# Kernel tuning notes

Hardware: AMD Instinct MI355X
Metric: run time of the kernel (lower is better)

## Reference

```python
import jax, jax.numpy as jnp
import numpy as np

NUM_EMBEDDINGS = 512
EMBEDDING_DIM = 64
COMMITMENT_COST = 0.25


def setup_inputs() -> dict:
    key = jax.random.key(0)
    k1, k2 = jax.random.split(key)
    inputs = jax.random.normal(k1, (64, 32, 32, EMBEDDING_DIM), dtype=jnp.float32)
    # nn.Embedding weight init: uniform(-1/K, 1/K)
    codebook = jax.random.uniform(
        k2, (NUM_EMBEDDINGS, EMBEDDING_DIM), dtype=jnp.float32,
        minval=-1.0 / NUM_EMBEDDINGS, maxval=1.0 / NUM_EMBEDDINGS)
    return {"inputs": inputs, "codebook": codebook}


def reference(inputs, codebook):
    D = codebook.shape[1]
    K = codebook.shape[0]
    flat = inputs.reshape(-1, D)  # [N, D]
    # Squared euclidean distances (argmin-equivalent to torch.cdist output)
    d2 = (jnp.sum(flat * flat, axis=1, keepdims=True)
          - 2.0 * (flat @ codebook.T)
          + jnp.sum(codebook * codebook, axis=1))  # [N, K]
    idx = jnp.argmin(d2, axis=1)  # [N]
    # Gather codebook rows (== one-hot @ codebook in the original)
    quantized = codebook[idx].reshape(inputs.shape)
    e_latent_loss = jnp.mean((jax.lax.stop_gradient(quantized) - inputs) ** 2)
    q_latent_loss = jnp.mean((quantized - jax.lax.stop_gradient(inputs)) ** 2)
    loss = q_latent_loss + COMMITMENT_COST * e_latent_loss
    # Straight-through estimator
    quantized_st = inputs + jax.lax.stop_gradient(quantized - inputs)
    # Perplexity from code usage histogram (== mean of one-hot encodings)
    n = flat.shape[0]
    avg_probs = jnp.zeros((K,), dtype=jnp.float32).at[idx].add(1.0) / n
    perplexity = jnp.exp(-jnp.sum(avg_probs * jnp.log(avg_probs + 1e-10)))
    encoding_indices = idx[:, None]  # [N, 1] to match torch unsqueeze(1)
    return (loss, quantized_st, perplexity, encoding_indices)
```

## Files before the change

### kernel.cpp

```cpp
#include <hip/hip_runtime.h>
#include <math.h>

#define K_EMB 512
#define DIM 64
#define NVEC 65536
#define OUT_LOSS 0
#define OUT_Q 1
#define OUT_PERP (1 + NVEC * DIM)
#define OUT_IDX (1 + NVEC * DIM + 1)
#define EPS2 1e-4f
#define FIX_CAP 32

typedef __attribute__((ext_vector_type(8))) short short8;
typedef __attribute__((ext_vector_type(4))) float float4v;


__device__ __forceinline__ unsigned short bf16_rn(float f) {
    unsigned u = __float_as_uint(f);
    return (unsigned short)((u + 0x7FFFu + ((u >> 16) & 1u)) >> 16);
}

__device__ __forceinline__ float np_pairwise8_sq(const float* v) {
    float r[8];
#pragma unroll
    for (int j = 0; j < 8; ++j) r[j] = __fmul_rn(v[j], v[j]);
#pragma unroll
    for (int i = 8; i < 64; i += 8) {
#pragma unroll
        for (int j = 0; j < 8; ++j) r[j] = __fadd_rn(r[j], __fmul_rn(v[i + j], v[i + j]));
    }
    return __fadd_rn(__fadd_rn(__fadd_rn(r[0], r[1]), __fadd_rn(r[2], r[3])),
                     __fadd_rn(__fadd_rn(r[4], r[5]), __fadd_rn(r[6], r[7])));
}

__global__ void vq_setup(const float* __restrict__ codebook, float* __restrict__ csq) {
    const int k = threadIdx.x;
    csq[k] = np_pairwise8_sq(codebook + (k << 6));
}

__global__ void vq_frag(const float* __restrict__ codebook, const float* __restrict__ csq,
                        unsigned short* __restrict__ ahi, unsigned short* __restrict__ alo,
                        float4* __restrict__ csqf) {
    const int id = blockIdx.x * 256 + threadIdx.x;
    const int t = id >> 7, step = (id >> 6) & 1, lane = id & 63;
    const int m = t * 16 + (lane & 15);
    const int kb = step * 32 + (lane >> 4) * 8;
    const float* src = codebook + (m << 6) + kb;
    short8 h, l;
#pragma unroll
    for (int j = 0; j < 8; ++j) {
        float f = src[j];
        unsigned short hv = bf16_rn(f);
        float lof = f - __uint_as_float(((unsigned)hv) << 16);
        h[j] = (short)hv;
        l[j] = (short)bf16_rn(lof);
    }
    const int fo = ((t * 2 + step) * 64 + lane) * 8;
    *(short8*)(ahi + fo) = h;
    *(short8*)(alo + fo) = l;
    if (step == 0) {
        const int k0 = t * 16 + (lane >> 4) * 4;
        csqf[t * 64 + lane] = make_float4(csq[k0], csq[k0 + 1], csq[k0 + 2], csq[k0 + 3]);
    }
}

__launch_bounds__(256, 4)
__global__ void vq_main(const float* __restrict__ inputs, const float* __restrict__ codebook,
                        const float* __restrict__ csq, const unsigned short* __restrict__ ahi,
                        const unsigned short* __restrict__ alo, const float4* __restrict__ csqf,
                        unsigned* __restrict__ hist, double* __restrict__ sse,
                        float* __restrict__ out) {
    __shared__ __align__(16) float s_x[128 * 68];
    __shared__ float s_A[128];
    __shared__ unsigned long long s_e[128];
    __shared__ unsigned s_h[512];
    __shared__ int s_fix[FIX_CAP];
    __shared__ int s_nfix;
    __shared__ float s_w[4];

    const int tid = threadIdx.x;
    const int wave = tid >> 6, lane = tid & 63;
    const int blk = blockIdx.x;
    const int vbase = blk * 128;

    if (tid == 0) s_nfix = 0;
    s_h[tid] = 0u; s_h[tid + 256] = 0u;

    {
        const float4* src = (const float4*)(inputs + ((size_t)vbase << 6));
#pragma unroll
        for (int it = 0; it < 8; ++it) {
            float4 v = src[it * 256 + tid];
            const int row = it * 16 + (tid >> 4), col = (tid & 15) * 4;
            *(float4*)&s_x[row * 68 + col] = v;
        }
    }
    __syncthreads();

    if (tid < 128) {
        const float* xr = &s_x[tid * 68];
        s_A[tid] = np_pairwise8_sq(xr);
    }
    __syncthreads();

    short8 bhi[2][2], blo[2][2];
    float Av[2];
#pragma unroll
    for (int vt = 0; vt < 2; ++vt) {
        const int vrow = wave * 32 + vt * 16 + (lane & 15);
        Av[vt] = s_A[vrow];
#pragma unroll
        for (int step = 0; step < 2; ++step) {
            const int kb = step * 32 + (lane >> 4) * 8;
            float4 f0 = *(const float4*)&s_x[vrow * 68 + kb];
            float4 f1 = *(const float4*)&s_x[vrow * 68 + kb + 4];
            const float fs[8] = {f0.x, f0.y, f0.z, f0.w, f1.x, f1.y, f1.z, f1.w};
            short8 h, l;
#pragma unroll
            for (int j = 0; j < 8; ++j) {
                unsigned short hv = bf16_rn(fs[j]);
                float lof = fs[j] - __uint_as_float(((unsigned)hv) << 16);
                h[j] = (short)hv;
                l[j] = (short)bf16_rn(lof);
            }
            bhi[vt][step] = h;
            blo[vt][step] = l;
        }
    }

    unsigned long long e1[2] = {~0ULL, ~0ULL}, e2[2] = {~0ULL, ~0ULL};

#pragma unroll 2
    for (int t = 0; t < 32; ++t) {
        const int fo0 = ((t * 2 + 0) * 64 + lane) * 8;
        const int fo1 = ((t * 2 + 1) * 64 + lane) * 8;
        short8 ah0 = *(const short8*)(ahi + fo0);
        short8 ah1 = *(const short8*)(ahi + fo1);
        short8 al0 = *(const short8*)(alo + fo0);
        short8 al1 = *(const short8*)(alo + fo1);
        float4 cs = csqf[t * 64 + lane];
        const float csr[4] = {cs.x, cs.y, cs.z, cs.w};
#pragma unroll
        for (int vt = 0; vt < 2; ++vt) {
            float4v acc = {0.f, 0.f, 0.f, 0.f};
            acc = __builtin_amdgcn_mfma_f32_16x16x32_bf16(ah0, bhi[vt][0], acc, 0, 0, 0);
            acc = __builtin_amdgcn_mfma_f32_16x16x32_bf16(ah1, bhi[vt][1], acc, 0, 0, 0);
            acc = __builtin_amdgcn_mfma_f32_16x16x32_bf16(ah0, blo[vt][0], acc, 0, 0, 0);
            acc = __builtin_amdgcn_mfma_f32_16x16x32_bf16(ah1, blo[vt][1], acc, 0, 0, 0);
            acc = __builtin_amdgcn_mfma_f32_16x16x32_bf16(al0, bhi[vt][0], acc, 0, 0, 0);
            acc = __builtin_amdgcn_mfma_f32_16x16x32_bf16(al1, bhi[vt][1], acc, 0, 0, 0);
#pragma unroll
            for (int r = 0; r < 4; ++r) {
                float d2 = __fadd_rn(__fsub_rn(Av[vt], __fmul_rn(2.0f, acc[r])), csr[r]);
                const unsigned k = (unsigned)(t * 16 + (lane >> 4) * 4 + r);
                unsigned long long e = ((unsigned long long)__float_as_uint(d2) << 32) | k;
                if (e < e1[vt]) { e2[vt] = e1[vt]; e1[vt] = e; }
                else if (e < e2[vt]) e2[vt] = e;
            }
        }
    }

#pragma unroll
    for (int vt = 0; vt < 2; ++vt) {
#pragma unroll
        for (int off = 16; off <= 32; off <<= 1) {
            unsigned long long o1 = __shfl_xor(e1[vt], off);
            unsigned long long o2 = __shfl_xor(e2[vt], off);
            if (o1 < e1[vt]) { e2[vt] = (e1[vt] < o2) ? e1[vt] : o2; e1[vt] = o1; }
            else if (o1 < e2[vt]) e2[vt] = o1;
        }
        if (lane < 16) {
            const int vloc = wave * 32 + vt * 16 + lane;
            s_e[vloc] = e1[vt];
            float b1 = __uint_as_float((unsigned)(e1[vt] >> 32));
            float b2 = __uint_as_float((unsigned)(e2[vt] >> 32));
            if (__fsub_rn(b2, b1) <= EPS2) {
                int pos = atomicAdd(&s_nfix, 1);
                if (pos < FIX_CAP) s_fix[pos] = vloc;
            }
        }
    }
    __syncthreads();

    {
        int nf = s_nfix; if (nf > FIX_CAP) nf = FIX_CAP;
        for (int f = wave; f < nf; f += 4) {
            const int vloc = s_fix[f];
            const float* xr = &s_x[vloc * 68];
            const float A = s_A[vloc];
            unsigned long long best = ~0ULL;
#pragma unroll 1
            for (int r8 = 0; r8 < 8; ++r8) {
                const int k = lane * 8 + r8;
                const float* c = codebook + (k << 6);
                float p[8] = {0.f, 0.f, 0.f, 0.f, 0.f, 0.f, 0.f, 0.f};
#pragma unroll
                for (int ii = 0; ii < 64; ii += 8)
#pragma unroll
                    for (int j = 0; j < 8; ++j)
                        p[j] = __builtin_fmaf(xr[ii + j], c[ii + j], p[j]);
                float dot = __fadd_rn(__fadd_rn(__fadd_rn(p[0], p[1]), __fadd_rn(p[2], p[3])),
                                      __fadd_rn(__fadd_rn(p[4], p[5]), __fadd_rn(p[6], p[7])));
                float d2 = __fadd_rn(__fsub_rn(A, __fmul_rn(2.0f, dot)), csq[k]);
                unsigned long long e = ((unsigned long long)__float_as_uint(d2) << 32) | (unsigned)k;
                if (e < best) best = e;
            }
#pragma unroll
            for (int off = 32; off > 0; off >>= 1) {
                unsigned long long o = __shfl_down(best, off);
                if (o < best) best = o;
            }
            if (lane == 0) s_e[vloc] = best;
        }
    }
    __syncthreads();

    if (tid < 128) {
        const unsigned kf = (unsigned)s_e[tid];
        out[OUT_IDX + vbase + tid] = (float)kf;
        atomicAdd(&s_h[kf], 1u);
    }
    {
        float4* dst = (float4*)(out + OUT_Q + ((size_t)vbase << 6));
        float es = 0.f;
#pragma unroll
        for (int it = 0; it < 8; ++it) {
            const int row = it * 16 + (tid >> 4), col = (tid & 15) * 4;
            const unsigned k = (unsigned)s_e[row];
            float4 qv = *(const float4*)(codebook + ((size_t)k << 6) + col);
            dst[it * 256 + tid] = qv;
            float4 xv = *(const float4*)&s_x[row * 68 + col];
            float d0 = qv.x - xv.x; es = __builtin_fmaf(d0, d0, es);
            float d1 = qv.y - xv.y; es = __builtin_fmaf(d1, d1, es);
            float d2 = qv.z - xv.z; es = __builtin_fmaf(d2, d2, es);
            float d3 = qv.w - xv.w; es = __builtin_fmaf(d3, d3, es);
        }
#pragma unroll
        for (int off = 32; off > 0; off >>= 1) es += __shfl_down(es, off);
        if (lane == 0) s_w[wave] = es;
    }
    __syncthreads();
    if (tid == 0) atomicAdd(sse, (double)(((s_w[0] + s_w[1]) + (s_w[2] + s_w[3]))));
    if (s_h[tid]) atomicAdd(&hist[tid], s_h[tid]);
    if (s_h[tid + 256]) atomicAdd(&hist[tid + 256], s_h[tid + 256]);
}

__global__ void vq_final(const unsigned* __restrict__ hist, const double* __restrict__ sse,
                         float* __restrict__ out) {
    __shared__ float s_wsm[8];
    const int k = threadIdx.x;
    float pr = (float)hist[k] / 65536.0f;
    float v = __fmul_rn(pr, logf(__fadd_rn(pr, 1e-10f)));
#pragma unroll
    for (int off = 32; off > 0; off >>= 1) v += __shfl_down(v, off);
    if ((k & 63) == 0) s_wsm[k >> 6] = v;
    __syncthreads();
    if (k == 0) {
        float S = 0.f;
#pragma unroll
        for (int i = 0; i < 8; ++i) S += s_wsm[i];
        out[OUT_PERP] = expf(-S);
        float m = (float)(*sse / 4194304.0);
        out[OUT_LOSS] = __fadd_rn(m, __fmul_rn(0.25f, m));
    }
}

extern "C" void kernel_launch(void* const* d_in, const int* in_sizes, int n_in,
                              void* d_out, int out_size, void* d_ws, size_t ws_size,
                              hipStream_t stream) {
    const float* inputs   = (const float*)d_in[0];
    const float* codebook = (const float*)d_in[1];
    float* out = (float*)d_out;
    float*          csq  = (float*)d_ws;
    double*         sse  = (double*)((char*)d_ws + 2048);
    unsigned*       hist = (unsigned*)((char*)d_ws + 2112);
    unsigned short* ahi  = (unsigned short*)((char*)d_ws + 4224);
    unsigned short* alo  = (unsigned short*)((char*)d_ws + 69760);
    float4*         csqf = (float4*)((char*)d_ws + 135296);

    hipMemsetAsync((char*)d_ws + 2048, 0, 2112, stream);
    vq_setup<<<1, 512, 0, stream>>>(codebook, csq);
    vq_frag<<<16, 256, 0, stream>>>(codebook, csq, ahi, alo, csqf);
    vq_main<<<512, 256, 0, stream>>>(inputs, codebook, csq, ahi, alo, csqf, hist, sse, out);
    vq_final<<<1, 512, 0, stream>>>(hist, sse, out);
}
```

Baseline: 151.5 us.

## Split codebook across waves, halve vectors per block, fold setup into frag kernel

Each block now handles 64 vectors instead of 128, and each wave scans one quarter of the codebook for all 64 vectors. Per-wave top-2 candidates are merged through shared memory. This doubles the grid to 1024 blocks for more parallelism and lowers shared memory per block. The setup kernel and the memset are folded into the frag kernel, which zeroes the histogram and the SSE accumulators itself. SSE is spread over 64 double slots to reduce atomic contention. The histogram now uses global atomics per vector instead of a shared-memory histogram, which may add contention.

```diff
diff --git a/kernel.cpp b/kernel.cpp
--- a/kernel.cpp
+++ b/kernel.cpp
@@ -9,7 +9,7 @@
 #define OUT_PERP (1 + NVEC * DIM)
 #define OUT_IDX (1 + NVEC * DIM + 1)
 #define EPS2 1e-4f
-#define FIX_CAP 32
+#define FIX_CAP 16
 
 typedef __attribute__((ext_vector_type(8))) short short8;
 typedef __attribute__((ext_vector_type(4))) float float4v;
@@ -33,14 +33,10 @@
                      __fadd_rn(__fadd_rn(r[4], r[5]), __fadd_rn(r[6], r[7])));
 }
 
-__global__ void vq_setup(const float* __restrict__ codebook, float* __restrict__ csq) {
-    const int k = threadIdx.x;
-    csq[k] = np_pairwise8_sq(codebook + (k << 6));
-}
-
-__global__ void vq_frag(const float* __restrict__ codebook, const float* __restrict__ csq,
+__global__ void vq_frag(const float* __restrict__ codebook, float* __restrict__ csq,
                         unsigned short* __restrict__ ahi, unsigned short* __restrict__ alo,
-                        float4* __restrict__ csqf) {
+                        float4* __restrict__ csqf, unsigned* __restrict__ hist,
+                        double* __restrict__ sse64) {
     const int id = blockIdx.x * 256 + threadIdx.x;
     const int t = id >> 7, step = (id >> 6) & 1, lane = id & 63;
     const int m = t * 16 + (lane & 15);
@@ -60,55 +56,57 @@
     *(short8*)(alo + fo) = l;
     if (step == 0) {
         const int k0 = t * 16 + (lane >> 4) * 4;
-        csqf[t * 64 + lane] = make_float4(csq[k0], csq[k0 + 1], csq[k0 + 2], csq[k0 + 3]);
-    }
+        csqf[t * 64 + lane] = make_float4(np_pairwise8_sq(codebook + (size_t)(k0 + 0) * 64),
+                                          np_pairwise8_sq(codebook + (size_t)(k0 + 1) * 64),
+                                          np_pairwise8_sq(codebook + (size_t)(k0 + 2) * 64),
+                                          np_pairwise8_sq(codebook + (size_t)(k0 + 3) * 64));
+    }
+    if (id < 512) {
+        csq[id] = np_pairwise8_sq(codebook + ((size_t)id << 6));
+        hist[id] = 0u;
+    }
+    if (id >= 512 && id < 576) sse64[id - 512] = 0.0;
 }
 
 __launch_bounds__(256, 4)
 __global__ void vq_main(const float* __restrict__ inputs, const float* __restrict__ codebook,
                         const float* __restrict__ csq, const unsigned short* __restrict__ ahi,
                         const unsigned short* __restrict__ alo, const float4* __restrict__ csqf,
-                        unsigned* __restrict__ hist, double* __restrict__ sse,
+                        unsigned* __restrict__ hist, double* __restrict__ sse64,
                         float* __restrict__ out) {
-    __shared__ __align__(16) float s_x[128 * 68];
-    __shared__ float s_A[128];
-    __shared__ unsigned long long s_e[128];
-    __shared__ unsigned s_h[512];
+    __shared__ __align__(16) float s_x[64 * 68];
+    __shared__ float s_A[64];
+    __shared__ unsigned long long s_t1[4][64];
+    __shared__ unsigned long long s_t2[4][64];
+    __shared__ unsigned long long s_e[64];
     __shared__ int s_fix[FIX_CAP];
     __shared__ int s_nfix;
     __shared__ float s_w[4];
 
     const int tid = threadIdx.x;
     const int wave = tid >> 6, lane = tid & 63;
-    const int blk = blockIdx.x;
-    const int vbase = blk * 128;
+    const int vbase = blockIdx.x * 64;
 
     if (tid == 0) s_nfix = 0;
-    s_h[tid] = 0u; s_h[tid + 256] = 0u;
 
     {
         const float4* src = (const float4*)(inputs + ((size_t)vbase << 6));
 #pragma unroll
-        for (int it = 0; it < 8; ++it) {
-            float4 v = src[it * 256 + tid];
-            const int row = it * 16 + (tid >> 4), col = (tid & 15) * 4;
-            *(float4*)&s_x[row * 68 + col] = v;
-        }
-    }
-    __syncthreads();
-
-    if (tid < 128) {
-        const float* xr = &s_x[tid * 68];
-        s_A[tid] = np_pairwise8_sq(xr);
-    }
-    __syncthreads();
-
-    short8 bhi[2][2], blo[2][2];
-    float Av[2];
-#pragma unroll
-    for (int vt = 0; vt < 2; ++vt) {
-        const int vrow = wave * 32 + vt * 16 + (lane & 15);
-        Av[vt] = s_A[vrow];
+        for (int i = 0; i < 4; ++i) {
+            const int f = i * 256 + tid;
+            float4 v = src[f];
+            *(float4*)&s_x[(f >> 4) * 68 + (f & 15) * 4] = v;
+        }
+    }
+    __syncthreads();
+
+    if (tid < 64) s_A[tid] = np_pairwise8_sq(&s_x[tid * 68]);
+    __syncthreads();
+
+    short8 bhi[4][2], blo[4][2];
+#pragma unroll
+    for (int vt = 0; vt < 4; ++vt) {
+        const int vrow = vt * 16 + (lane & 15);
 #pragma unroll
         for (int step = 0; step < 2; ++step) {
             const int kb = step * 32 + (lane >> 4) * 8;
@@ -128,10 +126,12 @@
         }
     }
 
-    unsigned long long e1[2] = {~0ULL, ~0ULL}, e2[2] = {~0ULL, ~0ULL};
+    unsigned long long e1[4] = {~0ULL, ~0ULL, ~0ULL, ~0ULL};
+    unsigned long long e2[4] = {~0ULL, ~0ULL, ~0ULL, ~0ULL};
 
 #pragma unroll 2
-    for (int t = 0; t < 32; ++t) {
+    for (int tt = 0; tt < 8; ++tt) {
+        const int t = wave * 8 + tt;
         const int fo0 = ((t * 2 + 0) * 64 + lane) * 8;
         const int fo1 = ((t * 2 + 1) * 64 + lane) * 8;
         short8 ah0 = *(const short8*)(ahi + fo0);
@@ -141,7 +141,7 @@
         float4 cs = csqf[t * 64 + lane];
         const float csr[4] = {cs.x, cs.y, cs.z, cs.w};
 #pragma unroll
-        for (int vt = 0; vt < 2; ++vt) {
+        for (int vt = 0; vt < 4; ++vt) {
             float4v acc = {0.f, 0.f, 0.f, 0.f};
             acc = __builtin_amdgcn_mfma_f32_16x16x32_bf16(ah0, bhi[vt][0], acc, 0, 0, 0);
             acc = __builtin_amdgcn_mfma_f32_16x16x32_bf16(ah1, bhi[vt][1], acc, 0, 0, 0);
@@ -149,9 +149,10 @@
             acc = __builtin_amdgcn_mfma_f32_16x16x32_bf16(ah1, blo[vt][1], acc, 0, 0, 0);
             acc = __builtin_amdgcn_mfma_f32_16x16x32_bf16(al0, bhi[vt][0], acc, 0, 0, 0);
             acc = __builtin_amdgcn_mfma_f32_16x16x32_bf16(al1, bhi[vt][1], acc, 0, 0, 0);
+            const float Avt = s_A[vt * 16 + (lane & 15)];
 #pragma unroll
             for (int r = 0; r < 4; ++r) {
-                float d2 = __fadd_rn(__fsub_rn(Av[vt], __fmul_rn(2.0f, acc[r])), csr[r]);
+                float d2 = __fadd_rn(__fsub_rn(Avt, __fmul_rn(2.0f, acc[r])), csr[r]);
                 const unsigned k = (unsigned)(t * 16 + (lane >> 4) * 4 + r);
                 unsigned long long e = ((unsigned long long)__float_as_uint(d2) << 32) | k;
                 if (e < e1[vt]) { e2[vt] = e1[vt]; e1[vt] = e; }
@@ -161,7 +162,7 @@
     }
 
 #pragma unroll
-    for (int vt = 0; vt < 2; ++vt) {
+    for (int vt = 0; vt < 4; ++vt) {
 #pragma unroll
         for (int off = 16; off <= 32; off <<= 1) {
             unsigned long long o1 = __shfl_xor(e1[vt], off);
@@ -170,14 +171,26 @@
             else if (o1 < e2[vt]) e2[vt] = o1;
         }
         if (lane < 16) {
-            const int vloc = wave * 32 + vt * 16 + lane;
-            s_e[vloc] = e1[vt];
-            float b1 = __uint_as_float((unsigned)(e1[vt] >> 32));
-            float b2 = __uint_as_float((unsigned)(e2[vt] >> 32));
-            if (__fsub_rn(b2, b1) <= EPS2) {
-                int pos = atomicAdd(&s_nfix, 1);
-                if (pos < FIX_CAP) s_fix[pos] = vloc;
-            }
+            s_t1[wave][vt * 16 + lane] = e1[vt];
+            s_t2[wave][vt * 16 + lane] = e2[vt];
+        }
+    }
+    __syncthreads();
+
+    if (tid < 64) {
+        unsigned long long E1 = ~0ULL, E2 = ~0ULL;
+#pragma unroll
+        for (int w = 0; w < 4; ++w) {
+            unsigned long long a = s_t1[w][tid], b = s_t2[w][tid];
+            if (a < E1) { E2 = (E1 < b) ? E1 : b; E1 = a; }
+            else if (a < E2) E2 = a;
+        }
+        s_e[tid] = E1;
+        float b1 = __uint_as_float((unsigned)(E1 >> 32));
+        float b2 = __uint_as_float((unsigned)(E2 >> 32));
+        if (__fsub_rn(b2, b1) <= EPS2) {
+            int pos = atomicAdd(&s_nfix, 1);
+            if (pos < FIX_CAP) s_fix[pos] = tid;
         }
     }
     __syncthreads();
@@ -215,20 +228,21 @@
     }
     __syncthreads();
 
-    if (tid < 128) {
+    if (tid < 64) {
         const unsigned kf = (unsigned)s_e[tid];
         out[OUT_IDX + vbase + tid] = (float)kf;
-        atomicAdd(&s_h[kf], 1u);
+        atomicAdd(&hist[kf], 1u);
     }
     {
         float4* dst = (float4*)(out + OUT_Q + ((size_t)vbase << 6));
         float es = 0.f;
 #pragma unroll
-        for (int it = 0; it < 8; ++it) {
-            const int row = it * 16 + (tid >> 4), col = (tid & 15) * 4;
+        for (int i = 0; i < 4; ++i) {
+            const int f = i * 256 + tid;
+            const int row = f >> 4, col = (f & 15) * 4;
             const unsigned k = (unsigned)s_e[row];
             float4 qv = *(const float4*)(codebook + ((size_t)k << 6) + col);
-            dst[it * 256 + tid] = qv;
+            dst[f] = qv;
             float4 xv = *(const float4*)&s_x[row * 68 + col];
             float d0 = qv.x - xv.x; es = __builtin_fmaf(d0, d0, es);
             float d1 = qv.y - xv.y; es = __builtin_fmaf(d1, d1, es);
@@ -240,12 +254,12 @@
         if (lane == 0) s_w[wave] = es;
     }
     __syncthreads();
-    if (tid == 0) atomicAdd(sse, (double)(((s_w[0] + s_w[1]) + (s_w[2] + s_w[3]))));
-    if (s_h[tid]) atomicAdd(&hist[tid], s_h[tid]);
-    if (s_h[tid + 256]) atomicAdd(&hist[tid + 256], s_h[tid + 256]);
-}
-
-__global__ void vq_final(const unsigned* __restrict__ hist, const double* __restrict__ sse,
+    if (tid == 0)
+        atomicAdd(&sse64[blockIdx.x & 63],
+                  (double)(((s_w[0] + s_w[1]) + (s_w[2] + s_w[3]))));
+}
+
+__global__ void vq_final(const unsigned* __restrict__ hist, const double* __restrict__ sse64,
                          float* __restrict__ out) {
     __shared__ float s_wsm[8];
     const int k = threadIdx.x;
@@ -260,7 +274,9 @@
 #pragma unroll
         for (int i = 0; i < 8; ++i) S += s_wsm[i];
         out[OUT_PERP] = expf(-S);
-        float m = (float)(*sse / 4194304.0);
+        double sv = 0.0;
+        for (int i = 0; i < 64; ++i) sv += sse64[i];
+        float m = (float)(sv / 4194304.0);
         out[OUT_LOSS] = __fadd_rn(m, __fmul_rn(0.25f, m));
     }
 }
@@ -271,16 +287,14 @@
     const float* inputs   = (const float*)d_in[0];
     const float* codebook = (const float*)d_in[1];
     float* out = (float*)d_out;
-    float*          csq  = (float*)d_ws;
-    double*         sse  = (double*)((char*)d_ws + 2048);
-    unsigned*       hist = (unsigned*)((char*)d_ws + 2112);
-    unsigned short* ahi  = (unsigned short*)((char*)d_ws + 4224);
-    unsigned short* alo  = (unsigned short*)((char*)d_ws + 69760);
-    float4*         csqf = (float4*)((char*)d_ws + 135296);
-
-    hipMemsetAsync((char*)d_ws + 2048, 0, 2112, stream);
-    vq_setup<<<1, 512, 0, stream>>>(codebook, csq);
-    vq_frag<<<16, 256, 0, stream>>>(codebook, csq, ahi, alo, csqf);
-    vq_main<<<512, 256, 0, stream>>>(inputs, codebook, csq, ahi, alo, csqf, hist, sse, out);
-    vq_final<<<1, 512, 0, stream>>>(hist, sse, out);
-}
+    float*          csq   = (float*)d_ws;
+    double*         sse64 = (double*)((char*)d_ws + 2048);
+    unsigned*       hist  = (unsigned*)((char*)d_ws + 2560);
+    unsigned short* ahi   = (unsigned short*)((char*)d_ws + 4608);
+    unsigned short* alo   = (unsigned short*)((char*)d_ws + 70144);
+    float4*         csqf  = (float4*)((char*)d_ws + 135680);
+
+    vq_frag<<<16, 256, 0, stream>>>(codebook, csq, ahi, alo, csqf, hist, sse64);
+    vq_main<<<1024, 256, 0, stream>>>(inputs, codebook, csq, ahi, alo, csqf, hist, sse64, out);
+    vq_final<<<1, 512, 0, stream>>>(hist, sse64, out);
+}
```

Result: slower. 155.1 us (+2.4%).
